# Optimization experiments

Measured on AMD Instinct MI355X. Metric: run time of the kernel, lower is better.

## Reference

```python
import jax, jax.numpy as jnp
import numpy as np

B, S, N = 8, 4, 64
ATOM_FDIM, BOND_FDIM, H = 133, 147, 300
DEPTH = 3


def setup_inputs() -> dict:
    key = jax.random.key(0)
    ks = jax.random.split(key, 9)
    f_atoms = jax.random.normal(ks[0], (B, S, N, ATOM_FDIM), dtype=jnp.float32)
    f_bonds = jax.random.uniform(ks[1], (B, S, N, N, BOND_FDIM), dtype=jnp.float32)
    adj = (jax.random.uniform(ks[2], (B, S, N, N)) < 0.3).astype(jnp.float32)
    def lin(k, fan_in, fan_out):
        return jax.random.normal(k, (fan_in, fan_out), dtype=jnp.float32) / np.sqrt(fan_in)
    return {
        'f_atoms': f_atoms,
        'f_bonds': f_bonds,
        'adj': adj,
        'W_i_atom': lin(ks[3], ATOM_FDIM, H),   # bias=False
        'W_i_bond': lin(ks[4], BOND_FDIM, H),   # bias=False
        'W_h_0': lin(ks[5], H, H),              # bias=False
        'W_h_1': lin(ks[6], H, H),              # bias=False
        'W_o': lin(ks[7], 3 * H, H),            # bias=True
        'b_o': jax.random.normal(ks[8], (H,), dtype=jnp.float32) * 0.01,
    }


def reference(f_atoms, f_bonds, adj, W_i_atom, W_i_bond, W_h_0, W_h_1, W_o, b_o):
    act = jax.nn.relu
    # atom / bond input embeddings
    input_atom = act(f_atoms @ W_i_atom)                        # [B,S,N,H]
    message_atom = input_atom
    input_bond = act((adj[..., None] * f_bonds) @ W_i_bond)     # [B,S,N,N,H]
    message_bond = input_bond
    for W_h in (W_h_0, W_h_1):  # depth-1 message-passing steps
        agg = message_bond.sum(axis=2) * jax.nn.sigmoid(message_bond.max(axis=2))  # [B,S,N,H]
        message_atom = message_atom + agg
        resonance = jnp.einsum('bsnd,bsmd->bsnm', message_atom, message_atom) * adj  # [B,S,N,N]
        # broadcast atom messages along edges, subtract reverse message
        mb = adj[..., None] * message_atom[:, :, None, :, :] - message_bond  # [B,S,N,N,H]
        mb = jnp.swapaxes(mb, 2, 3)  # permute(0,1,3,2,4)
        mb = act(input_bond + mb @ W_h)
        message_bond = mb * jax.nn.softmax(resonance, axis=2)[..., None]
    agg = message_bond.sum(axis=2) * jax.nn.sigmoid(message_bond.max(axis=2))
    a_input = jnp.concatenate([agg, message_atom, input_atom], axis=-1)  # [B,S,N,3H]
    atom_hiddens = act(a_input @ W_o + b_o)  # [B,S,N,H]
    return atom_hiddens, message_bond
```

## Files before the change

### kernel.cpp

```cpp
#include <hip/hip_runtime.h>
#include <hip/hip_bf16.h>
#include <math.h>

#define Bc 8
#define Sc 4
#define Nc 64
#define AF 133
#define BFD 147
#define Hc 300
#define BS (Bc*Sc)
#define ROWS (BS*Nc)
#define EDGES (BS*Nc*Nc)
#define BSLICE 19456
#define BHALF  9728

typedef float f32x4 __attribute__((ext_vector_type(4)));
typedef short bf16x8 __attribute__((ext_vector_type(8)));
typedef float f32x4v __attribute__((ext_vector_type(4)));
typedef f32x4v f32x4u __attribute__((aligned(4)));
union U4 { uint4 u; bf16x8 v; };

__device__ __forceinline__ float reluf(float x){ return fmaxf(x, 0.f); }
__device__ __forceinline__ float b2f(unsigned short u){ union{unsigned int i;float f;}v; v.i = ((unsigned int)u)<<16; return v.f; }
__device__ __forceinline__ unsigned short f2b(float f){ __hip_bfloat16 h = __float2bfloat16(f); return *reinterpret_cast<unsigned short*>(&h); }
__device__ __forceinline__ void split2(float x, unsigned short &hi, unsigned short &lo){
    unsigned short h = f2b(x);
    float r = x - b2f(h);
    hi = h; lo = f2b(r);
}

typedef __attribute__((address_space(1))) const unsigned int* gas1_t;
typedef __attribute__((address_space(3))) unsigned int* las3_t;
__device__ __forceinline__ void gload_lds16(const void* g, void* l){
    __builtin_amdgcn_global_load_lds((gas1_t)g, (las3_t)l, 16, 0, 0);
}

__device__ __forceinline__ void bar_only(){
    __builtin_amdgcn_sched_barrier(0);
    asm volatile("" ::: "memory");
    __builtin_amdgcn_s_barrier();
    asm volatile("" ::: "memory");
    __builtin_amdgcn_sched_barrier(0);
}
__device__ __forceinline__ void bar_drain(){
    __builtin_amdgcn_sched_barrier(0);
    asm volatile("s_waitcnt vmcnt(0) lgkmcnt(0)" ::: "memory");
    __builtin_amdgcn_s_barrier();
    asm volatile("" ::: "memory");
    __builtin_amdgcn_sched_barrier(0);
}

__global__ __launch_bounds__(320) void k_atom_embed(const float* __restrict__ f_atoms,
        const float* __restrict__ W, float* __restrict__ input_atom, float* __restrict__ message_atom){
    __shared__ float x[AF];
    int row = blockIdx.x;
    const float* fr = f_atoms + (size_t)row*AF;
    for (int d = threadIdx.x; d < AF; d += blockDim.x) x[d] = fr[d];
    __syncthreads();
    int h = threadIdx.x;
    if (h < Hc){
        float acc = 0.f;
        for (int d = 0; d < AF; ++d) acc = fmaf(x[d], W[d*Hc + h], acc);
        float v = reluf(acc);
        input_atom[(size_t)row*Hc + h] = v;
        message_atom[(size_t)row*Hc + h] = v;
    }
}

__global__ __launch_bounds__(256) void k_prep_wp2(const float* __restrict__ W, int K, int NKT,
        unsigned short* __restrict__ WP){
    int idx = blockIdx.x*256 + threadIdx.x;
    if (idx >= NKT*BSLICE) return;
    int j  = idx & 7;
    int l  = (idx >> 3) & 63;
    int ct = (idx >> 9) % 19;
    int rem = idx / BHALF;
    int hl = rem & 1;
    int kt = rem >> 1;
    int col = ct*16 + (l & 15);
    int k   = kt*32 + (l >> 4)*8 + j;
    float v = (col < Hc && k < K) ? W[k*Hc + col] : 0.f;
    unsigned short hi, lo; split2(v, hi, lo);
    WP[idx] = hl ? lo : hi;
}

template<int MODE>
__global__ __launch_bounds__(1024) void k_gemm_t(
        const float* __restrict__ Asrc,
        const unsigned short* __restrict__ WP,
        const float* __restrict__ ma,
        const float* __restrict__ adj,
        const float* __restrict__ sm,
        const float* __restrict__ ib,
        float* __restrict__ dst,
        float* __restrict__ aggb)
{
    constexpr int NKT  = (MODE != 0) ? 10 : 5;
    constexpr int ASTR = (MODE != 0) ? 300 : BFD;

    __shared__ unsigned short sAhi[4096];
    __shared__ unsigned short sAlo[4096];
    __shared__ unsigned short sB[BSLICE];
    __shared__ int s_eOut[128];
    __shared__ int s_eRev[128];
    __shared__ float s_adjRev[128];
    __shared__ int s_aAtom[128];

    const int t = threadIdx.x;
    const int bs0 = blockIdx.x >> 5;
    const int mp0 = blockIdx.x & 31;

    if constexpr (MODE == 1){
        if (t < 128){
            int r = t;
            int bs = bs0, kk = mp0;
            int s1 = 64-kk, s2 = 127-2*kk, s3 = 128-kk;
            int a, b;
            if (r < s1){ a = kk; b = kk + r; }
            else if (r < s2){ a = kk+1 + (r - s1); b = kk; }
            else if (r < s3){ a = 63-kk; b = 63-kk + (r - s2); }
            else { a = 64-kk + (r - s3); b = 63-kk; }
            int eo = (bs*64 + a)*64 + b;
            int er = (bs*64 + b)*64 + a;
            s_eOut[r] = eo; s_eRev[r] = er; s_aAtom[r] = bs*64 + a;
            s_adjRev[r] = adj[er];
        }
        __syncthreads();
    }

    const int rt_b = t >> 7;
    const int q_b  = (t >> 5) & 3;
    const int li_b = (t >> 1) & 15;
    const int half = t & 1;
    const int brow = rt_b*16 + li_b;
    const int koff = q_b*8 + 4*half;
    const float* aRow;
    const float* mRow = nullptr;
    float adjR = 0.f;
    if constexpr (MODE == 1){
        aRow = Asrc + (size_t)s_eRev[brow]*ASTR;
        mRow = ma + (size_t)s_aAtom[brow]*Hc;
        adjR = s_adjRev[brow];
    } else if constexpr (MODE == 2){
        int n = brow & 63, cc = brow >> 6;
        int eR = (bs0*64 + (2*mp0 + cc))*64 + n;
        aRow = Asrc + (size_t)eR*ASTR;
        mRow = ma + (size_t)(bs0*64 + n)*Hc;
        adjR = adj[eR];
    } else {
        int n = brow & 63, cc = brow >> 6;
        int e = (bs0*64 + n)*64 + (2*mp0 + cc);
        aRow = Asrc + (size_t)e*ASTR;
        adjR = adj[e];
    }

    float pm[4], pa[4];
    auto prefetchA = [&](int kt){
        int k0 = kt*32 + koff;
        if constexpr (MODE != 0){
            if (k0 <= 296){
                float4 v = *(const float4*)(aRow + k0);
                float4 w = *(const float4*)(mRow + k0);
                pm[0]=v.x; pm[1]=v.y; pm[2]=v.z; pm[3]=v.w;
                pa[0]=w.x; pa[1]=w.y; pa[2]=w.z; pa[3]=w.w;
            }
        } else {
            if (k0 + 3 < BFD){
                f32x4u v = *(const f32x4u*)(aRow + k0);
                pm[0]=v.x; pm[1]=v.y; pm[2]=v.z; pm[3]=v.w;
            } else {
                #pragma unroll
                for (int j = 0; j < 4; ++j){
                    int k = k0 + j;
                    pm[j] = (k < BFD) ? aRow[k] : 0.f;
                }
            }
        }
    };
    auto buildA = [&](int kt){
        int k0 = kt*32 + koff;
        float xv[4];
        if constexpr (MODE != 0){
            if (k0 <= 296){
                #pragma unroll
                for (int j = 0; j < 4; ++j) xv[j] = fmaf(adjR, pa[j], -pm[j]);
            } else { xv[0]=xv[1]=xv[2]=xv[3]=0.f; }
        } else {
            #pragma unroll
            for (int j = 0; j < 4; ++j) xv[j] = adjR * pm[j];
        }
        unsigned short h0,l0,h1,l1,h2,l2,h3,l3;
        split2(xv[0],h0,l0); split2(xv[1],h1,l1);
        split2(xv[2],h2,l2); split2(xv[3],h3,l3);
        uint2 hw, lw;
        hw.x = (unsigned int)h0 | ((unsigned int)h1<<16);
        hw.y = (unsigned int)h2 | ((unsigned int)h3<<16);
        lw.x = (unsigned int)l0 | ((unsigned int)l1<<16);
        lw.y = (unsigned int)l2 | ((unsigned int)l3<<16);
        *(uint2*)&sAhi[4*t] = hw;
        *(uint2*)&sAlo[4*t] = lw;
    };
    auto copyB = [&](int kt){
        const unsigned short* src = WP + (size_t)kt*BSLICE;
        #pragma unroll
        for (int rep = 0; rep < 3; ++rep){
            int i = t + rep*1024;
            if (i < BSLICE/8)
                gload_lds16(src + (size_t)i*8, &sB[i*8]);
        }
    };

    const int wv = t >> 6, lane = t & 63;
    const int li = lane & 15, quad = lane >> 4;
    const int rg = wv & 3;
    const int cg = wv >> 2;
    const int c0 = cg*5;
    const int myC = (cg < 3) ? 5 : 4;

    f32x4 acc[5][2];
    #pragma unroll
    for (int c = 0; c < 5; ++c){ acc[c][0] = (f32x4){0,0,0,0}; acc[c][1] = (f32x4){0,0,0,0}; }

    prefetchA(0);

    if constexpr (MODE != 0){
        #pragma unroll
        for (int c = 0; c < 5; ++c){
            if (c < myC){
                int h = (c0 + c)*16 + li;
                if (h < Hc){
                    #pragma unroll
                    for (int r2 = 0; r2 < 2; ++r2)
                        #pragma unroll
                        for (int i = 0; i < 4; ++i){
                            int row = (2*rg + r2)*16 + quad*4 + i;
                            int e;
                            if constexpr (MODE == 1) e = s_eOut[row];
                            else e = (bs0*64 + (row & 63))*64 + (2*mp0 + (row >> 6));
                            acc[c][r2][i] = ib[(size_t)e*Hc + h];
                        }
                }
            }
        }
    }

    for (int kt = 0; kt < NKT; ++kt){
        if (kt) bar_only();
        copyB(kt);
        buildA(kt);
        bar_drain();
        if (kt+1 < NKT) prefetchA(kt+1);
        __builtin_amdgcn_s_setprio(1);
        U4 a0h, a0l, a1h, a1l;
        a0h.u = *(const uint4*)&sAhi[((2*rg  )*64 + lane)*8];
        a0l.u = *(const uint4*)&sAlo[((2*rg  )*64 + lane)*8];
        a1h.u = *(const uint4*)&sAhi[((2*rg+1)*64 + lane)*8];
        a1l.u = *(const uint4*)&sAlo[((2*rg+1)*64 + lane)*8];
        #pragma unroll
        for (int c = 0; c < 5; ++c){
            if (c < myC){
                U4 bh, bl;
                bh.u = *(const uint4*)&sB[        (c0+c)*512 + lane*8];
                bl.u = *(const uint4*)&sB[BHALF + (c0+c)*512 + lane*8];
                acc[c][0] = __builtin_amdgcn_mfma_f32_16x16x32_bf16(a0h.v, bl.v, acc[c][0], 0,0,0);
                acc[c][0] = __builtin_amdgcn_mfma_f32_16x16x32_bf16(a0l.v, bh.v, acc[c][0], 0,0,0);
                acc[c][0] = __builtin_amdgcn_mfma_f32_16x16x32_bf16(a0h.v, bh.v, acc[c][0], 0,0,0);
                acc[c][1] = __builtin_amdgcn_mfma_f32_16x16x32_bf16(a1h.v, bl.v, acc[c][1], 0,0,0);
                acc[c][1] = __builtin_amdgcn_mfma_f32_16x16x32_bf16(a1l.v, bh.v, acc[c][1], 0,0,0);
                acc[c][1] = __builtin_amdgcn_mfma_f32_16x16x32_bf16(a1h.v, bh.v, acc[c][1], 0,0,0);
            }
        }
        __builtin_amdgcn_s_setprio(0);
    }

    if constexpr (MODE == 1){
        int eO[2][4]; float smv[2][4];
        #pragma unroll
        for (int r2 = 0; r2 < 2; ++r2)
            #pragma unroll
            for (int i = 0; i < 4; ++i){
                int row = (2*rg + r2)*16 + quad*4 + i;
                int e = s_eOut[row];
                eO[r2][i] = e;
                smv[r2][i] = sm[e];
            }
        #pragma unroll
        for (int c = 0; c < 5; ++c){
            if (c >= myC) continue;
            int h = (c0 + c)*16 + li;
            if (h >= Hc) continue;
            #pragma unroll
            for (int r2 = 0; r2 < 2; ++r2)
                #pragma unroll
                for (int i = 0; i < 4; ++i){
                    size_t off = (size_t)eO[r2][i]*Hc + h;
                    dst[off] = reluf(acc[c][r2][i]) * smv[r2][i];
                }
        }
    } else {
        __syncthreads();
        float* sRedS = (float*)sB;
        float* sRedM = sRedS + 16*304;
        int eO[2][4]; float smv[2][4];
        #pragma unroll
        for (int r2 = 0; r2 < 2; ++r2)
            #pragma unroll
            for (int i = 0; i < 4; ++i){
                int row = (2*rg + r2)*16 + quad*4 + i;
                int e = (bs0*64 + (row & 63))*64 + (2*mp0 + (row >> 6));
                eO[r2][i] = e;
                if constexpr (MODE == 2) smv[r2][i] = sm[e];
            }
        #pragma unroll
        for (int c = 0; c < 5; ++c){
            float s8 = 0.f, m8 = -INFINITY;
            int h = (c0 + c)*16 + li;
            if (c < myC && h < Hc){
                #pragma unroll
                for (int r2 = 0; r2 < 2; ++r2)
                    #pragma unroll
                    for (int i = 0; i < 4; ++i){
                        float v = reluf(acc[c][r2][i]);
                        if constexpr (MODE == 2) v *= smv[r2][i];
                        dst[(size_t)eO[r2][i]*Hc + h] = v;
                        s8 += v; m8 = fmaxf(m8, v);
                    }
            }
            s8 += __shfl_xor(s8, 16, 64); s8 += __shfl_xor(s8, 32, 64);
            m8 = fmaxf(m8, __shfl_xor(m8, 16, 64)); m8 = fmaxf(m8, __shfl_xor(m8, 32, 64));
            if (c < myC && quad == 0){
                sRedS[wv*304 + (c0 + c)*16 + li] = s8;
                sRedM[wv*304 + (c0 + c)*16 + li] = m8;
            }
        }
        __syncthreads();
        if (t < 608){
            int cc = t / 304, h = t - cc*304;
            if (h < Hc){
                int ct = h >> 4;
                int cgf = (ct < 15) ? (ct/5) : 3;
                int w0 = (cgf << 2) + 2*cc;
                float s = sRedS[w0*304 + h] + sRedS[(w0+1)*304 + h];
                float m = fmaxf(sRedM[w0*304 + h], sRedM[(w0+1)*304 + h]);
                float agg = s * (1.f/(1.f + expf(-m)));
                size_t o = (size_t)(bs0*64 + 2*mp0 + cc)*Hc + h;
                if constexpr (MODE == 0) aggb[o] += agg;
                else                     aggb[o]  = agg;
            }
        }
    }
}

__global__ __launch_bounds__(256) void k_ma_add(float* __restrict__ ma, const float* __restrict__ aggb){
    int i = blockIdx.x*256 + threadIdx.x;
    if (i < ROWS*Hc/4){
        float4 a = ((const float4*)aggb)[i];
        float4 v = ((float4*)ma)[i];
        v.x += a.x; v.y += a.y; v.z += a.z; v.w += a.w;
        ((float4*)ma)[i] = v;
    }
}

__global__ __launch_bounds__(320) void k_agg(const float* __restrict__ message_bond,
        float* __restrict__ message_atom, float* __restrict__ agg_out, int final_mode){
    int t = threadIdx.x;
    int r = t / 80, c = t - r*80;
    if (c >= 75) return;
    int row = blockIdx.x*4 + r;
    int bs = row >> 6, m = row & 63;
    size_t base = ((size_t)(bs*Nc)*Nc + m)*(size_t)Hc + (size_t)c*4;
    float4 s  = {0.f, 0.f, 0.f, 0.f};
    float4 mx = {-INFINITY, -INFINITY, -INFINITY, -INFINITY};
    #pragma unroll 4
    for (int n = 0; n < Nc; ++n){
        float4 v = *(const float4*)(message_bond + base + (size_t)n*Nc*Hc);
        s.x += v.x; s.y += v.y; s.z += v.z; s.w += v.w;
        mx.x = fmaxf(mx.x, v.x); mx.y = fmaxf(mx.y, v.y);
        mx.z = fmaxf(mx.z, v.z); mx.w = fmaxf(mx.w, v.w);
    }
    float4 agg;
    agg.x = s.x * (1.f/(1.f + expf(-mx.x)));
    agg.y = s.y * (1.f/(1.f + expf(-mx.y)));
    agg.z = s.z * (1.f/(1.f + expf(-mx.z)));
    agg.w = s.w * (1.f/(1.f + expf(-mx.w)));
    size_t o = (size_t)row*Hc + (size_t)c*4;
    if (final_mode){
        *(float4*)(agg_out + o) = agg;
    } else {
        float4 cur = *(const float4*)(message_atom + o);
        cur.x += agg.x; cur.y += agg.y; cur.z += agg.z; cur.w += agg.w;
        *(float4*)(message_atom + o) = cur;
    }
}

__global__ __launch_bounds__(256) void k_resonance_softmax(const float* __restrict__ message_atom,
        const float* __restrict__ adj, float* __restrict__ sm){
    int bs = blockIdx.x >> 6, m = blockIdx.x & 63;
    __shared__ float am[Hc];
    __shared__ float res[Nc];
    for (int d = threadIdx.x; d < Hc; d += blockDim.x)
        am[d] = message_atom[((size_t)(bs*Nc)+m)*Hc + d];
    __syncthreads();
    int wave = threadIdx.x >> 6, lane = threadIdx.x & 63;
    for (int n = wave; n < Nc; n += 4){
        const float* man = message_atom + ((size_t)(bs*Nc)+n)*Hc;
        float acc = 0.f;
        for (int d = lane; d < Hc; d += 64) acc = fmaf(man[d], am[d], acc);
        #pragma unroll
        for (int off = 32; off > 0; off >>= 1) acc += __shfl_xor(acc, off, 64);
        if (lane == 0) res[n] = acc * adj[((size_t)(bs*Nc)+n)*Nc + m];
    }
    __syncthreads();
    if (threadIdx.x < Nc){
        float v = res[threadIdx.x];
        float mx = v;
        #pragma unroll
        for (int off = 32; off > 0; off >>= 1) mx = fmaxf(mx, __shfl_xor(mx, off, 64));
        float e = expf(v - mx);
        float ssum = e;
        #pragma unroll
        for (int off = 32; off > 0; off >>= 1) ssum += __shfl_xor(ssum, off, 64);
        sm[((size_t)(bs*Nc)+threadIdx.x)*Nc + m] = e / ssum;
    }
}

#define R7 4
__global__ __launch_bounds__(320) void k_output(const float* __restrict__ agg,
        const float* __restrict__ message_atom, const float* __restrict__ input_atom,
        const float* __restrict__ W_o, const float* __restrict__ b_o, float* __restrict__ out){
    __shared__ float xin[R7][3*Hc];
    int r0 = blockIdx.x * R7;
    for (int idx = threadIdx.x; idx < R7*3*Hc; idx += blockDim.x){
        int r = idx / (3*Hc), k = idx - r*(3*Hc);
        int row = r0 + r;
        float v;
        if (k < Hc)           v = agg[(size_t)row*Hc + k];
        else if (k < 2*Hc)    v = message_atom[(size_t)row*Hc + (k - Hc)];
        else                  v = input_atom[(size_t)row*Hc + (k - 2*Hc)];
        xin[r][k] = v;
    }
    __syncthreads();
    int h = threadIdx.x;
    if (h < Hc){
        float acc[R7];
        #pragma unroll
        for (int r=0;r<R7;r++) acc[r] = b_o[h];
        for (int d = 0; d < 3*Hc; ++d){
            float w = W_o[d*Hc + h];
            #pragma unroll
            for (int r=0;r<R7;r++) acc[r] = fmaf(xin[r][d], w, acc[r]);
        }
        #pragma unroll
        for (int r=0;r<R7;r++) out[(size_t)(r0+r)*Hc + h] = reluf(acc[r]);
    }
}

extern "C" void kernel_launch(void* const* d_in, const int* in_sizes, int n_in,
                              void* d_out, int out_size, void* d_ws, size_t ws_size,
                              hipStream_t stream){
    const float* f_atoms  = (const float*)d_in[0];
    const float* f_bonds  = (const float*)d_in[1];
    const float* adj      = (const float*)d_in[2];
    const float* W_i_atom = (const float*)d_in[3];
    const float* W_i_bond = (const float*)d_in[4];
    const float* W_h0     = (const float*)d_in[5];
    const float* W_h1     = (const float*)d_in[6];
    const float* W_o      = (const float*)d_in[7];
    const float* b_o      = (const float*)d_in[8];

    float* out = (float*)d_out;
    float* atom_hiddens = out;
    float* mb_out = out + (size_t)ROWS*Hc;

    float* wsf = (float*)d_ws;
    float* input_atom   = wsf; wsf += (size_t)ROWS*Hc;
    float* message_atom = wsf; wsf += (size_t)ROWS*Hc;
    float* sm           = wsf; wsf += (size_t)EDGES;
    float* aggb         = wsf; wsf += (size_t)ROWS*Hc;
    float* ib           = wsf; wsf += (size_t)EDGES*Hc;
    unsigned short* wsu = (unsigned short*)wsf;
    unsigned short* WP0 = wsu; wsu += 10*BSLICE;
    unsigned short* WP1 = wsu; wsu += 10*BSLICE;
    unsigned short* WPb = wsu; wsu += 5*BSLICE;

    size_t used = (size_t)((char*)wsu - (char*)d_ws);
    used = (used + 255) & ~(size_t)255;
    float* mbx = nullptr;
    if (ws_size >= used + (size_t)EDGES*Hc*sizeof(float))
        mbx = (float*)((char*)d_ws + used);

    k_atom_embed<<<ROWS, 320, 0, stream>>>(f_atoms, W_i_atom, input_atom, message_atom);
    k_prep_wp2<<<(10*BSLICE + 255)/256, 256, 0, stream>>>(W_h0, Hc, 10, WP0);
    k_prep_wp2<<<(10*BSLICE + 255)/256, 256, 0, stream>>>(W_h1, Hc, 10, WP1);
    k_prep_wp2<<<(5*BSLICE + 255)/256, 256, 0, stream>>>(W_i_bond, BFD, 5, WPb);
    k_gemm_t<0><<<BS*32, 1024, 0, stream>>>(f_bonds, WPb, nullptr, adj, nullptr, nullptr, ib, message_atom);
    k_resonance_softmax<<<ROWS, 256, 0, stream>>>(message_atom, adj, sm);
    if (mbx){
        k_gemm_t<2><<<BS*32, 1024, 0, stream>>>(ib, WP0, message_atom, adj, sm, ib, mbx, aggb);
        k_ma_add<<<(ROWS*Hc/4 + 255)/256, 256, 0, stream>>>(message_atom, aggb);
        k_resonance_softmax<<<ROWS, 256, 0, stream>>>(message_atom, adj, sm);
        k_gemm_t<2><<<BS*32, 1024, 0, stream>>>(mbx, WP1, message_atom, adj, sm, ib, mb_out, aggb);
        k_output<<<ROWS/R7, 320, 0, stream>>>(aggb, message_atom, input_atom, W_o, b_o, atom_hiddens);
    } else {
        float* agg_out = ib;
        k_gemm_t<2><<<BS*32, 1024, 0, stream>>>(ib, WP0, message_atom, adj, sm, ib, mb_out, aggb);
        k_ma_add<<<(ROWS*Hc/4 + 255)/256, 256, 0, stream>>>(message_atom, aggb);
        k_resonance_softmax<<<ROWS, 256, 0, stream>>>(message_atom, adj, sm);
        k_gemm_t<1><<<BS*32, 1024, 0, stream>>>(mb_out, WP1, message_atom, adj, sm, ib, mb_out, nullptr);
        k_agg<<<ROWS/4, 320, 0, stream>>>(mb_out, nullptr, agg_out, 1);
        k_output<<<ROWS/R7, 320, 0, stream>>>(agg_out, message_atom, input_atom, W_o, b_o, atom_hiddens);
    }
}
```

Baseline: 738.7 us.

## Shrink edge-GEMM tiles to 64 rows per block and merge weight prep

The main edge GEMM kernel now runs 512-thread blocks that each handle one 64-edge column (one output atom) instead of two, doubling the grid and making the aggregation reduction per block simpler. The in-place reverse-edge path moves to a separate kernel with the old 1024-thread layout. The three weight-packing launches are merged into one, and the atom-embed and output kernels now process more rows per block to reuse weight loads. The smaller tiles aim for better occupancy and less launch overhead, at the cost of loading the B weights more often per edge.

```diff
diff --git a/kernel.cpp b/kernel.cpp
--- a/kernel.cpp
+++ b/kernel.cpp
@@ -50,31 +50,48 @@
     __builtin_amdgcn_sched_barrier(0);
 }
 
+#define RA 4
 __global__ __launch_bounds__(320) void k_atom_embed(const float* __restrict__ f_atoms,
         const float* __restrict__ W, float* __restrict__ input_atom, float* __restrict__ message_atom){
-    __shared__ float x[AF];
-    int row = blockIdx.x;
-    const float* fr = f_atoms + (size_t)row*AF;
-    for (int d = threadIdx.x; d < AF; d += blockDim.x) x[d] = fr[d];
+    __shared__ float x[RA][AF];
+    int r0 = blockIdx.x * RA;
+    for (int idx = threadIdx.x; idx < RA*AF; idx += blockDim.x){
+        int r = idx / AF, d = idx - r*AF;
+        x[r][d] = f_atoms[(size_t)(r0+r)*AF + d];
+    }
     __syncthreads();
     int h = threadIdx.x;
     if (h < Hc){
-        float acc = 0.f;
-        for (int d = 0; d < AF; ++d) acc = fmaf(x[d], W[d*Hc + h], acc);
-        float v = reluf(acc);
-        input_atom[(size_t)row*Hc + h] = v;
-        message_atom[(size_t)row*Hc + h] = v;
-    }
-}
-
-__global__ __launch_bounds__(256) void k_prep_wp2(const float* __restrict__ W, int K, int NKT,
+        float acc[RA];
+        #pragma unroll
+        for (int r = 0; r < RA; ++r) acc[r] = 0.f;
+        for (int d = 0; d < AF; ++d){
+            float w = W[d*Hc + h];
+            #pragma unroll
+            for (int r = 0; r < RA; ++r) acc[r] = fmaf(x[r][d], w, acc[r]);
+        }
+        #pragma unroll
+        for (int r = 0; r < RA; ++r){
+            float v = reluf(acc[r]);
+            input_atom[(size_t)(r0+r)*Hc + h] = v;
+            message_atom[(size_t)(r0+r)*Hc + h] = v;
+        }
+    }
+}
+
+__global__ __launch_bounds__(256) void k_prep_all(const float* __restrict__ W_h0,
+        const float* __restrict__ W_h1, const float* __restrict__ W_ib,
         unsigned short* __restrict__ WP){
     int idx = blockIdx.x*256 + threadIdx.x;
-    if (idx >= NKT*BSLICE) return;
-    int j  = idx & 7;
-    int l  = (idx >> 3) & 63;
-    int ct = (idx >> 9) % 19;
-    int rem = idx / BHALF;
+    if (idx >= 25*BSLICE) return;
+    const float* W; int K; int lidx;
+    if (idx < 10*BSLICE){ W = W_h0; K = Hc; lidx = idx; }
+    else if (idx < 20*BSLICE){ W = W_h1; K = Hc; lidx = idx - 10*BSLICE; }
+    else { W = W_ib; K = BFD; lidx = idx - 20*BSLICE; }
+    int j  = lidx & 7;
+    int l  = (lidx >> 3) & 63;
+    int ct = (lidx >> 9) % 19;
+    int rem = lidx / BHALF;
     int hl = rem & 1;
     int kt = rem >> 1;
     int col = ct*16 + (l & 15);
@@ -85,7 +102,7 @@
 }
 
 template<int MODE>
-__global__ __launch_bounds__(1024) void k_gemm_t(
+__global__ __launch_bounds__(512) void k_gemm_c(
         const float* __restrict__ Asrc,
         const unsigned short* __restrict__ WP,
         const float* __restrict__ ma,
@@ -98,58 +115,28 @@
     constexpr int NKT  = (MODE != 0) ? 10 : 5;
     constexpr int ASTR = (MODE != 0) ? 300 : BFD;
 
-    __shared__ unsigned short sAhi[4096];
-    __shared__ unsigned short sAlo[4096];
+    __shared__ unsigned short sAhi[2048];
+    __shared__ unsigned short sAlo[2048];
     __shared__ unsigned short sB[BSLICE];
-    __shared__ int s_eOut[128];
-    __shared__ int s_eRev[128];
-    __shared__ float s_adjRev[128];
-    __shared__ int s_aAtom[128];
 
     const int t = threadIdx.x;
-    const int bs0 = blockIdx.x >> 5;
-    const int mp0 = blockIdx.x & 31;
-
-    if constexpr (MODE == 1){
-        if (t < 128){
-            int r = t;
-            int bs = bs0, kk = mp0;
-            int s1 = 64-kk, s2 = 127-2*kk, s3 = 128-kk;
-            int a, b;
-            if (r < s1){ a = kk; b = kk + r; }
-            else if (r < s2){ a = kk+1 + (r - s1); b = kk; }
-            else if (r < s3){ a = 63-kk; b = 63-kk + (r - s2); }
-            else { a = 64-kk + (r - s3); b = 63-kk; }
-            int eo = (bs*64 + a)*64 + b;
-            int er = (bs*64 + b)*64 + a;
-            s_eOut[r] = eo; s_eRev[r] = er; s_aAtom[r] = bs*64 + a;
-            s_adjRev[r] = adj[er];
-        }
-        __syncthreads();
-    }
-
-    const int rt_b = t >> 7;
-    const int q_b  = (t >> 5) & 3;
+    const int bs0  = blockIdx.x >> 6;
+    const int mcol = blockIdx.x & 63;
+
     const int li_b = (t >> 1) & 15;
-    const int half = t & 1;
-    const int brow = rt_b*16 + li_b;
-    const int koff = q_b*8 + 4*half;
+    const int brow = (t >> 7)*16 + li_b;
+    const int koff = ((t >> 5) & 3)*8 + (t & 1)*4;
+
     const float* aRow;
     const float* mRow = nullptr;
-    float adjR = 0.f;
-    if constexpr (MODE == 1){
-        aRow = Asrc + (size_t)s_eRev[brow]*ASTR;
-        mRow = ma + (size_t)s_aAtom[brow]*Hc;
-        adjR = s_adjRev[brow];
-    } else if constexpr (MODE == 2){
-        int n = brow & 63, cc = brow >> 6;
-        int eR = (bs0*64 + (2*mp0 + cc))*64 + n;
+    float adjR;
+    if constexpr (MODE == 2){
+        int eR = (bs0*64 + mcol)*64 + brow;
         aRow = Asrc + (size_t)eR*ASTR;
-        mRow = ma + (size_t)(bs0*64 + n)*Hc;
+        mRow = ma + (size_t)(bs0*64 + brow)*Hc;
         adjR = adj[eR];
     } else {
-        int n = brow & 63, cc = brow >> 6;
-        int e = (bs0*64 + n)*64 + (2*mp0 + cc);
+        int e = (bs0*64 + brow)*64 + mcol;
         aRow = Asrc + (size_t)e*ASTR;
         adjR = adj[e];
     }
@@ -203,8 +190,8 @@
     auto copyB = [&](int kt){
         const unsigned short* src = WP + (size_t)kt*BSLICE;
         #pragma unroll
-        for (int rep = 0; rep < 3; ++rep){
-            int i = t + rep*1024;
+        for (int rep = 0; rep < 5; ++rep){
+            int i = t + rep*512;
             if (i < BSLICE/8)
                 gload_lds16(src + (size_t)i*8, &sB[i*8]);
         }
@@ -212,10 +199,10 @@
 
     const int wv = t >> 6, lane = t & 63;
     const int li = lane & 15, quad = lane >> 4;
-    const int rg = wv & 3;
-    const int cg = wv >> 2;
-    const int c0 = cg*5;
-    const int myC = (cg < 3) ? 5 : 4;
+    const int rowg = wv & 1;
+    const int colg = wv >> 1;
+    const int c0 = colg*5;
+    const int myC = (colg < 3) ? 5 : 4;
 
     f32x4 acc[5][2];
     #pragma unroll
@@ -223,25 +210,22 @@
 
     prefetchA(0);
 
-    if constexpr (MODE != 0){
-        #pragma unroll
-        for (int c = 0; c < 5; ++c){
-            if (c < myC){
-                int h = (c0 + c)*16 + li;
-                if (h < Hc){
-                    #pragma unroll
-                    for (int r2 = 0; r2 < 2; ++r2)
-                        #pragma unroll
-                        for (int i = 0; i < 4; ++i){
-                            int row = (2*rg + r2)*16 + quad*4 + i;
-                            int e;
-                            if constexpr (MODE == 1) e = s_eOut[row];
-                            else e = (bs0*64 + (row & 63))*64 + (2*mp0 + (row >> 6));
-                            acc[c][r2][i] = ib[(size_t)e*Hc + h];
-                        }
+    if constexpr (MODE == 2){
+        #pragma unroll
+        for (int r2 = 0; r2 < 2; ++r2)
+            #pragma unroll
+            for (int i = 0; i < 4; ++i){
+                int row = (2*rowg + r2)*16 + quad*4 + i;
+                int e = (bs0*64 + row)*64 + mcol;
+                const float* ibr = ib + (size_t)e*Hc;
+                #pragma unroll
+                for (int c = 0; c < 5; ++c){
+                    if (c < myC){
+                        int h = (c0 + c)*16 + li;
+                        if (h < Hc) acc[c][r2][i] = ibr[h];
+                    }
                 }
             }
-        }
     }
 
     for (int kt = 0; kt < NKT; ++kt){
@@ -252,10 +236,10 @@
         if (kt+1 < NKT) prefetchA(kt+1);
         __builtin_amdgcn_s_setprio(1);
         U4 a0h, a0l, a1h, a1l;
-        a0h.u = *(const uint4*)&sAhi[((2*rg  )*64 + lane)*8];
-        a0l.u = *(const uint4*)&sAlo[((2*rg  )*64 + lane)*8];
-        a1h.u = *(const uint4*)&sAhi[((2*rg+1)*64 + lane)*8];
-        a1l.u = *(const uint4*)&sAlo[((2*rg+1)*64 + lane)*8];
+        a0h.u = *(const uint4*)&sAhi[((2*rowg  )*64 + lane)*8];
+        a0l.u = *(const uint4*)&sAlo[((2*rowg  )*64 + lane)*8];
+        a1h.u = *(const uint4*)&sAhi[((2*rowg+1)*64 + lane)*8];
+        a1l.u = *(const uint4*)&sAlo[((2*rowg+1)*64 + lane)*8];
         #pragma unroll
         for (int c = 0; c < 5; ++c){
             if (c < myC){
@@ -273,82 +257,212 @@
         __builtin_amdgcn_s_setprio(0);
     }
 
-    if constexpr (MODE == 1){
-        int eO[2][4]; float smv[2][4];
-        #pragma unroll
-        for (int r2 = 0; r2 < 2; ++r2)
+    __syncthreads();
+    float* sRedS = (float*)sB;
+    float* sRedM = sRedS + 8*304;
+    float s8[5], m8[5];
+    #pragma unroll
+    for (int c = 0; c < 5; ++c){ s8[c] = 0.f; m8[c] = -INFINITY; }
+    #pragma unroll
+    for (int r2 = 0; r2 < 2; ++r2)
+        #pragma unroll
+        for (int i = 0; i < 4; ++i){
+            int row = (2*rowg + r2)*16 + quad*4 + i;
+            int e = (bs0*64 + row)*64 + mcol;
+            float smr = 0.f;
+            if constexpr (MODE == 2) smr = sm[e];
+            float* drow = dst + (size_t)e*Hc;
             #pragma unroll
-            for (int i = 0; i < 4; ++i){
-                int row = (2*rg + r2)*16 + quad*4 + i;
-                int e = s_eOut[row];
-                eO[r2][i] = e;
-                smv[r2][i] = sm[e];
-            }
-        #pragma unroll
-        for (int c = 0; c < 5; ++c){
-            if (c >= myC) continue;
+            for (int c = 0; c < 5; ++c){
+                if (c < myC){
+                    int h = (c0 + c)*16 + li;
+                    if (h < Hc){
+                        float v = reluf(acc[c][r2][i]);
+                        if constexpr (MODE == 2) v *= smr;
+                        drow[h] = v;
+                        s8[c] += v; m8[c] = fmaxf(m8[c], v);
+                    }
+                }
+            }
+        }
+    #pragma unroll
+    for (int c = 0; c < 5; ++c){
+        float s = s8[c], m = m8[c];
+        s += __shfl_xor(s, 16, 64); s += __shfl_xor(s, 32, 64);
+        m = fmaxf(m, __shfl_xor(m, 16, 64)); m = fmaxf(m, __shfl_xor(m, 32, 64));
+        if (c < myC && quad == 0){
+            sRedS[wv*304 + (c0 + c)*16 + li] = s;
+            sRedM[wv*304 + (c0 + c)*16 + li] = m;
+        }
+    }
+    __syncthreads();
+    if (t < Hc){
+        int h = t;
+        int ct = h >> 4;
+        int colgf = (ct < 15) ? (ct/5) : 3;
+        int w0 = colgf << 1;
+        float s = sRedS[w0*304 + h] + sRedS[(w0+1)*304 + h];
+        float m = fmaxf(sRedM[w0*304 + h], sRedM[(w0+1)*304 + h]);
+        float agg = s * (1.f/(1.f + expf(-m)));
+        size_t o = (size_t)(bs0*64 + mcol)*Hc + h;
+        if constexpr (MODE == 0) aggb[o] += agg;
+        else                     aggb[o]  = agg;
+    }
+}
+
+__global__ __launch_bounds__(1024) void k_gemm_p(
+        const float* __restrict__ Asrc,
+        const unsigned short* __restrict__ WP,
+        const float* __restrict__ ma,
+        const float* __restrict__ adj,
+        const float* __restrict__ sm,
+        const float* __restrict__ ib,
+        float* __restrict__ dst)
+{
+    constexpr int NKT  = 10;
+    constexpr int ASTR = 300;
+    __shared__ unsigned short sAhi[4096];
+    __shared__ unsigned short sAlo[4096];
+    __shared__ unsigned short sB[BSLICE];
+    __shared__ int s_eOut[128];
+    __shared__ int s_eRev[128];
+    __shared__ float s_adjRev[128];
+    __shared__ int s_aAtom[128];
+
+    const int t = threadIdx.x;
+    if (t < 128){
+        int r = t;
+        int bs = blockIdx.x >> 5, kk = blockIdx.x & 31;
+        int s1 = 64-kk, s2 = 127-2*kk, s3 = 128-kk;
+        int a, b;
+        if (r < s1){ a = kk; b = kk + r; }
+        else if (r < s2){ a = kk+1 + (r - s1); b = kk; }
+        else if (r < s3){ a = 63-kk; b = 63-kk + (r - s2); }
+        else { a = 64-kk + (r - s3); b = 63-kk; }
+        int eo = (bs*64 + a)*64 + b;
+        int er = (bs*64 + b)*64 + a;
+        s_eOut[r] = eo; s_eRev[r] = er; s_aAtom[r] = bs*64 + a;
+        s_adjRev[r] = adj[er];
+    }
+    __syncthreads();
+
+    const int rt_b = t >> 7;
+    const int li_b = (t >> 1) & 15;
+    const int brow = rt_b*16 + li_b;
+    const int koff = ((t >> 5) & 3)*8 + (t & 1)*4;
+    const float* aRow = Asrc + (size_t)s_eRev[brow]*ASTR;
+    const float* mRow = ma + (size_t)s_aAtom[brow]*Hc;
+    float adjR = s_adjRev[brow];
+
+    float pm[4], pa[4];
+    auto prefetchA = [&](int kt){
+        int k0 = kt*32 + koff;
+        if (k0 <= 296){
+            float4 v = *(const float4*)(aRow + k0);
+            float4 w = *(const float4*)(mRow + k0);
+            pm[0]=v.x; pm[1]=v.y; pm[2]=v.z; pm[3]=v.w;
+            pa[0]=w.x; pa[1]=w.y; pa[2]=w.z; pa[3]=w.w;
+        }
+    };
+    auto buildA = [&](int kt){
+        int k0 = kt*32 + koff;
+        float xv[4];
+        if (k0 <= 296){
+            #pragma unroll
+            for (int j = 0; j < 4; ++j) xv[j] = fmaf(adjR, pa[j], -pm[j]);
+        } else { xv[0]=xv[1]=xv[2]=xv[3]=0.f; }
+        unsigned short h0,l0,h1,l1,h2,l2,h3,l3;
+        split2(xv[0],h0,l0); split2(xv[1],h1,l1);
+        split2(xv[2],h2,l2); split2(xv[3],h3,l3);
+        uint2 hw, lw;
+        hw.x = (unsigned int)h0 | ((unsigned int)h1<<16);
+        hw.y = (unsigned int)h2 | ((unsigned int)h3<<16);
+        lw.x = (unsigned int)l0 | ((unsigned int)l1<<16);
+        lw.y = (unsigned int)l2 | ((unsigned int)l3<<16);
+        *(uint2*)&sAhi[4*t] = hw;
+        *(uint2*)&sAlo[4*t] = lw;
+    };
+    auto copyB = [&](int kt){
+        const unsigned short* src = WP + (size_t)kt*BSLICE;
+        #pragma unroll
+        for (int rep = 0; rep < 3; ++rep){
+            int i = t + rep*1024;
+            if (i < BSLICE/8)
+                gload_lds16(src + (size_t)i*8, &sB[i*8]);
+        }
+    };
+
+    const int wv = t >> 6, lane = t & 63;
+    const int li = lane & 15, quad = lane >> 4;
+    const int rg = wv & 3;
+    const int cg = wv >> 2;
+    const int c0 = cg*5;
+    const int myC = (cg < 3) ? 5 : 4;
+
+    f32x4 acc[5][2];
+    #pragma unroll
+    for (int c = 0; c < 5; ++c){ acc[c][0] = (f32x4){0,0,0,0}; acc[c][1] = (f32x4){0,0,0,0}; }
+
+    prefetchA(0);
+    #pragma unroll
+    for (int c = 0; c < 5; ++c){
+        if (c < myC){
             int h = (c0 + c)*16 + li;
-            if (h >= Hc) continue;
-            #pragma unroll
-            for (int r2 = 0; r2 < 2; ++r2)
-                #pragma unroll
-                for (int i = 0; i < 4; ++i){
-                    size_t off = (size_t)eO[r2][i]*Hc + h;
-                    dst[off] = reluf(acc[c][r2][i]) * smv[r2][i];
-                }
-        }
-    } else {
-        __syncthreads();
-        float* sRedS = (float*)sB;
-        float* sRedM = sRedS + 16*304;
-        int eO[2][4]; float smv[2][4];
-        #pragma unroll
-        for (int r2 = 0; r2 < 2; ++r2)
-            #pragma unroll
-            for (int i = 0; i < 4; ++i){
-                int row = (2*rg + r2)*16 + quad*4 + i;
-                int e = (bs0*64 + (row & 63))*64 + (2*mp0 + (row >> 6));
-                eO[r2][i] = e;
-                if constexpr (MODE == 2) smv[r2][i] = sm[e];
-            }
-        #pragma unroll
-        for (int c = 0; c < 5; ++c){
-            float s8 = 0.f, m8 = -INFINITY;
-            int h = (c0 + c)*16 + li;
-            if (c < myC && h < Hc){
+            if (h < Hc){
                 #pragma unroll
                 for (int r2 = 0; r2 < 2; ++r2)
                     #pragma unroll
                     for (int i = 0; i < 4; ++i){
-                        float v = reluf(acc[c][r2][i]);
-                        if constexpr (MODE == 2) v *= smv[r2][i];
-                        dst[(size_t)eO[r2][i]*Hc + h] = v;
-                        s8 += v; m8 = fmaxf(m8, v);
+                        int row = (2*rg + r2)*16 + quad*4 + i;
+                        acc[c][r2][i] = ib[(size_t)s_eOut[row]*Hc + h];
                     }
             }
-            s8 += __shfl_xor(s8, 16, 64); s8 += __shfl_xor(s8, 32, 64);
-            m8 = fmaxf(m8, __shfl_xor(m8, 16, 64)); m8 = fmaxf(m8, __shfl_xor(m8, 32, 64));
-            if (c < myC && quad == 0){
-                sRedS[wv*304 + (c0 + c)*16 + li] = s8;
-                sRedM[wv*304 + (c0 + c)*16 + li] = m8;
-            }
-        }
-        __syncthreads();
-        if (t < 608){
-            int cc = t / 304, h = t - cc*304;
-            if (h < Hc){
-                int ct = h >> 4;
-                int cgf = (ct < 15) ? (ct/5) : 3;
-                int w0 = (cgf << 2) + 2*cc;
-                float s = sRedS[w0*304 + h] + sRedS[(w0+1)*304 + h];
-                float m = fmaxf(sRedM[w0*304 + h], sRedM[(w0+1)*304 + h]);
-                float agg = s * (1.f/(1.f + expf(-m)));
-                size_t o = (size_t)(bs0*64 + 2*mp0 + cc)*Hc + h;
-                if constexpr (MODE == 0) aggb[o] += agg;
-                else                     aggb[o]  = agg;
-            }
-        }
-    }
+        }
+    }
+
+    for (int kt = 0; kt < NKT; ++kt){
+        if (kt) bar_only();
+        copyB(kt);
+        buildA(kt);
+        bar_drain();
+        if (kt+1 < NKT) prefetchA(kt+1);
+        U4 a0h, a0l, a1h, a1l;
+        a0h.u = *(const uint4*)&sAhi[((2*rg  )*64 + lane)*8];
+        a0l.u = *(const uint4*)&sAlo[((2*rg  )*64 + lane)*8];
+        a1h.u = *(const uint4*)&sAhi[((2*rg+1)*64 + lane)*8];
+        a1l.u = *(const uint4*)&sAlo[((2*rg+1)*64 + lane)*8];
+        #pragma unroll
+        for (int c = 0; c < 5; ++c){
+            if (c < myC){
+                U4 bh, bl;
+                bh.u = *(const uint4*)&sB[        (c0+c)*512 + lane*8];
+                bl.u = *(const uint4*)&sB[BHALF + (c0+c)*512 + lane*8];
+                acc[c][0] = __builtin_amdgcn_mfma_f32_16x16x32_bf16(a0h.v, bl.v, acc[c][0], 0,0,0);
+                acc[c][0] = __builtin_amdgcn_mfma_f32_16x16x32_bf16(a0l.v, bh.v, acc[c][0], 0,0,0);
+                acc[c][0] = __builtin_amdgcn_mfma_f32_16x16x32_bf16(a0h.v, bh.v, acc[c][0], 0,0,0);
+                acc[c][1] = __builtin_amdgcn_mfma_f32_16x16x32_bf16(a1h.v, bl.v, acc[c][1], 0,0,0);
+                acc[c][1] = __builtin_amdgcn_mfma_f32_16x16x32_bf16(a1l.v, bh.v, acc[c][1], 0,0,0);
+                acc[c][1] = __builtin_amdgcn_mfma_f32_16x16x32_bf16(a1h.v, bh.v, acc[c][1], 0,0,0);
+            }
+        }
+    }
+
+    #pragma unroll
+    for (int r2 = 0; r2 < 2; ++r2)
+        #pragma unroll
+        for (int i = 0; i < 4; ++i){
+            int row = (2*rg + r2)*16 + quad*4 + i;
+            int e = s_eOut[row];
+            float smr = sm[e];
+            float* drow = dst + (size_t)e*Hc;
+            #pragma unroll
+            for (int c = 0; c < 5; ++c){
+                if (c < myC){
+                    int h = (c0 + c)*16 + li;
+                    if (h < Hc) drow[h] = reluf(acc[c][r2][i]) * smr;
+                }
+            }
+        }
 }
 
 __global__ __launch_bounds__(256) void k_ma_add(float* __restrict__ ma, const float* __restrict__ aggb){
@@ -424,7 +538,7 @@
     }
 }
 
-#define R7 4
+#define R7 8
 __global__ __launch_bounds__(320) void k_output(const float* __restrict__ agg,
         const float* __restrict__ message_atom, const float* __restrict__ input_atom,
         const float* __restrict__ W_o, const float* __restrict__ b_o, float* __restrict__ out){
@@ -489,24 +603,22 @@
     if (ws_size >= used + (size_t)EDGES*Hc*sizeof(float))
         mbx = (float*)((char*)d_ws + used);
 
-    k_atom_embed<<<ROWS, 320, 0, stream>>>(f_atoms, W_i_atom, input_atom, message_atom);
-    k_prep_wp2<<<(10*BSLICE + 255)/256, 256, 0, stream>>>(W_h0, Hc, 10, WP0);
-    k_prep_wp2<<<(10*BSLICE + 255)/256, 256, 0, stream>>>(W_h1, Hc, 10, WP1);
-    k_prep_wp2<<<(5*BSLICE + 255)/256, 256, 0, stream>>>(W_i_bond, BFD, 5, WPb);
-    k_gemm_t<0><<<BS*32, 1024, 0, stream>>>(f_bonds, WPb, nullptr, adj, nullptr, nullptr, ib, message_atom);
+    k_atom_embed<<<ROWS/RA, 320, 0, stream>>>(f_atoms, W_i_atom, input_atom, message_atom);
+    k_prep_all<<<(25*BSLICE + 255)/256, 256, 0, stream>>>(W_h0, W_h1, W_i_bond, WP0);
+    k_gemm_c<0><<<BS*64, 512, 0, stream>>>(f_bonds, WPb, nullptr, adj, nullptr, nullptr, ib, message_atom);
     k_resonance_softmax<<<ROWS, 256, 0, stream>>>(message_atom, adj, sm);
     if (mbx){
-        k_gemm_t<2><<<BS*32, 1024, 0, stream>>>(ib, WP0, message_atom, adj, sm, ib, mbx, aggb);
+        k_gemm_c<2><<<BS*64, 512, 0, stream>>>(ib, WP0, message_atom, adj, sm, ib, mbx, aggb);
         k_ma_add<<<(ROWS*Hc/4 + 255)/256, 256, 0, stream>>>(message_atom, aggb);
         k_resonance_softmax<<<ROWS, 256, 0, stream>>>(message_atom, adj, sm);
-        k_gemm_t<2><<<BS*32, 1024, 0, stream>>>(mbx, WP1, message_atom, adj, sm, ib, mb_out, aggb);
+        k_gemm_c<2><<<BS*64, 512, 0, stream>>>(mbx, WP1, message_atom, adj, sm, ib, mb_out, aggb);
         k_output<<<ROWS/R7, 320, 0, stream>>>(aggb, message_atom, input_atom, W_o, b_o, atom_hiddens);
     } else {
         float* agg_out = ib;
-        k_gemm_t<2><<<BS*32, 1024, 0, stream>>>(ib, WP0, message_atom, adj, sm, ib, mb_out, aggb);
+        k_gemm_c<2><<<BS*64, 512, 0, stream>>>(ib, WP0, message_atom, adj, sm, ib, mb_out, aggb);
         k_ma_add<<<(ROWS*Hc/4 + 255)/256, 256, 0, stream>>>(message_atom, aggb);
         k_resonance_softmax<<<ROWS, 256, 0, stream>>>(message_atom, adj, sm);
-        k_gemm_t<1><<<BS*32, 1024, 0, stream>>>(mb_out, WP1, message_atom, adj, sm, ib, mb_out, nullptr);
+        k_gemm_p<<<BS*32, 1024, 0, stream>>>(mb_out, WP1, message_atom, adj, sm, ib, mb_out);
         k_agg<<<ROWS/4, 320, 0, stream>>>(mb_out, nullptr, agg_out, 1);
         k_output<<<ROWS/R7, 320, 0, stream>>>(agg_out, message_atom, input_atom, W_o, b_o, atom_hiddens);
     }
```

Result: slower. 770.9 us (+4.4%).
